# Optimization experiments

Measured on AMD Instinct MI355X. Metric: run time of the kernel, lower is better.

## Reference

```python
import jax, jax.numpy as jnp
import numpy as np
from jax import lax

KSIZE, STRIDE, RATE, SOFTMAX_SCALE = 3, 1, 2, 10.0


def extract_patches(x, k, stride):
    # x: [B,C,H,W] -> [B,C,k,k,oh,ow]; torch-style zero 'same' padding
    B, C, H, W = x.shape
    oh, ow = -(-H // stride), -(-W // stride)
    ph = max(0, (oh - 1) * stride + k - H)
    pw = max(0, (ow - 1) * stride + k - W)
    x = jnp.pad(x, ((0, 0), (0, 0), (ph // 2, ph - ph // 2), (pw // 2, pw - pw // 2)))
    cols = [x[:, :, i:i + (oh - 1) * stride + 1:stride, j:j + (ow - 1) * stride + 1:stride]
            for i in range(k) for j in range(k)]
    return jnp.stack(cols, axis=2).reshape(B, C, k, k, oh, ow)


def setup_inputs():
    key = jax.random.key(0)
    kf, kb = jax.random.split(key)
    f = jax.random.normal(kf, (2, 128, 128, 128), dtype=jnp.float32)
    b = jax.random.normal(kb, (2, 128, 128, 128), dtype=jnp.float32)
    mask = jnp.zeros((2, 1, 512, 512), dtype=jnp.float32)
    mask = mask.at[:, :, 128:384, 128:384].set(1.0)  # central hole: bg patches unavailable
    return {"f": f, "b": b, "mask": mask}


def reference(f, b, mask):
    B, C, H, W = b.shape
    kernel = 2 * RATE
    # raw background patches used for reconstruction (stride = rate*stride)
    raw = extract_patches(b, kernel, RATE * STRIDE)            # [B,C,4,4,Hb,Wb]
    Hb, Wb = raw.shape[-2:]
    L = Hb * Wb
    raw_w = raw.transpose(0, 4, 5, 1, 2, 3).reshape(B, L, C, kernel, kernel)
    # nearest 1/rate downsample (integer rate -> strided slice)
    fs = f[:, :, ::RATE, ::RATE]
    bs = b[:, :, ::RATE, ::RATE]
    Hf, Wf = fs.shape[-2:]
    # matching patches from downsampled background, L2-normalized per patch
    wp = extract_patches(bs, KSIZE, STRIDE)                    # [B,C,3,3,Hb,Wb]
    w = wp.transpose(0, 4, 5, 1, 2, 3).reshape(B, L, C, KSIZE, KSIZE)
    norm = jnp.sqrt(jnp.sum(w * w, axis=(2, 3, 4), keepdims=True))
    w_normed = w / jnp.maximum(norm, 1e-4)
    # mask -> per-patch validity (original uses batch element 0 only)
    ms = mask[:, :, ::4 * RATE, ::4 * RATE]                    # [B,1,Hb,Wb]
    mp = extract_patches(ms, KSIZE, STRIDE)[0]                 # [1,3,3,Hb,Wb]
    mm = (jnp.mean(mp, axis=(0, 1, 2)).reshape(-1) == 0.0).astype(f.dtype)
    mm = mm.reshape(1, L, 1, 1)
    # similarity scores: per-image conv2d of fg with bg patches == patch einsum
    fp = extract_patches(fs, KSIZE, STRIDE)                    # [B,C,3,3,Hf,Wf]
    yi = jnp.einsum('bcpqhw,blcpq->blhw', fp, w_normed)        # [B,L,Hf,Wf]
    yi = yi * mm
    yi = jax.nn.softmax(yi * SOFTMAX_SCALE, axis=1)
    yi = yi * mm
    # argmax offsets relative to reference coordinates (int_bs == int_fs here)
    off = jnp.argmax(yi, axis=1)                               # [B,Hf,Wf]
    h_ref = jnp.arange(Hf)[None, :, None]
    w_ref = jnp.arange(Wf)[None, None, :]
    offsets = jnp.stack([off // Wf - h_ref, off % Wf - w_ref], axis=1)  # [B,2,Hf,Wf]
    # reconstruction: conv_transpose2d(yi, raw_wi, stride=rate, padding=1) / 4
    w_ct = jnp.flip(raw_w.transpose(0, 2, 1, 3, 4), axis=(-2, -1))      # [B,C,L,4,4]
    pad = kernel - 1 - 1  # transpose-conv padding=1 -> conv pad k-1-1
    def ct(a, wk):
        return lax.conv_general_dilated(a[None], wk, (1, 1),
                                        ((pad, pad), (pad, pad)),
                                        lhs_dilation=(RATE, RATE),
                                        dimension_numbers=('NCHW', 'OIHW', 'NCHW'))[0]
    y = jax.vmap(ct)(yi, w_ct) / 4.0                           # [B,C,H,W]
    return y, offsets
```

## Files before the change

kernel.cpp:

```cpp
#include <hip/hip_runtime.h>
#include <hip/hip_bf16.h>
#include <cstdint>

#define B_  2
#define C_  128
#define HH  128
#define WW  128
#define L_  4096
#define K1  1152
#define M2  2048
#define NPAD 3072
#define NCAND 16
#define MARGIN 0.15f
#define PCUT 5e-4f
#define MAXC 512

typedef __attribute__((ext_vector_type(8))) short bf16x8s;
typedef __attribute__((ext_vector_type(4))) float f32x4;
typedef __attribute__((ext_vector_type(2))) float f32x2;
using bf16 = __hip_bfloat16;

__device__ inline float bf16bits2f(unsigned short s) {
  uint32_t u = ((uint32_t)s) << 16;
  return __builtin_bit_cast(float, u);
}
__device__ inline unsigned short f2bf16bits(float x) {
  uint32_t u = __builtin_bit_cast(uint32_t, x);
  u += 0x7fffu + ((u >> 16) & 1u);
  return (unsigned short)(u >> 16);
}

__device__ inline uint8_t fp8_encode(float v) {
  uint32_t s = (__builtin_bit_cast(uint32_t, v) >> 24) & 0x80u;
  float av = fabsf(v);
  uint32_t byte;
  if (av >= 0.015625f) {
    uint32_t bits = __builtin_bit_cast(uint32_t, av);
    uint32_t mant = bits & 0x7fffffu;
    uint32_t E = bits >> 23;
    uint32_t m3 = (mant + 0x7ffffu + ((mant >> 20) & 1u)) >> 20;
    if (m3 == 8u) { m3 = 0u; E++; }
    int e8 = (int)E - 120;
    if (e8 > 15) { e8 = 15; m3 = 6; }
    byte = ((uint32_t)e8 << 3) | m3;
  } else {
    byte = (uint32_t)(av * 512.f + 0.5f);
  }
  return (uint8_t)(s | byte);
}

#if __has_builtin(__builtin_amdgcn_cvt_pk_f32_fp8)
#define FP8PK(d, hi) __builtin_amdgcn_cvt_pk_f32_fp8((d), (hi))
#else
__device__ inline f32x2 FP8PK(uint32_t d, bool hi) {
  uint32_t b0 = hi ? ((d >> 16) & 0xffu) : (d & 0xffu);
  uint32_t b1 = hi ? (d >> 24) : ((d >> 8) & 0xffu);
  f32x2 r;
  r.x = __builtin_bit_cast(float, ((b0 & 0x80u) << 24) | ((b0 & 0x7fu) << 20)) * 0x1p120f;
  r.y = __builtin_bit_cast(float, ((b1 & 0x80u) << 24) | ((b1 & 0x7fu) << 20)) * 0x1p120f;
  return r;
}
#endif

__device__ inline void gload_lds16(const void* g, void* l) {
  auto gp = reinterpret_cast<const __attribute__((address_space(1))) uint32_t*>(
      reinterpret_cast<uintptr_t>(g));
  auto lp = reinterpret_cast<__attribute__((address_space(3))) uint32_t*>(
      reinterpret_cast<uintptr_t>(l));
  __builtin_amdgcn_global_load_lds(gp, lp, 16, 0, 0);
}

__global__ void compute_mm_k(const float* __restrict__ mask, float* __restrict__ mm) {
  int l = blockIdx.x * 256 + threadIdx.x;
  if (l >= L_) return;
  int i = l >> 6, j = l & 63;
  float s = 0.f;
  for (int p = -1; p <= 1; ++p)
    for (int q = -1; q <= 1; ++q) {
      int y = i + p, x = j + q;
      if ((unsigned)y < 64u && (unsigned)x < 64u)
        s += mask[(size_t)(8 * y) * 512 + 8 * x];
    }
  mm[l] = (s == 0.f) ? 1.f : 0.f;
}

__global__ __launch_bounds__(256) void compact_k(const float* __restrict__ mm,
                                                 int* __restrict__ vlist,
                                                 int* __restrict__ vmap,
                                                 int* __restrict__ meta) {
  __shared__ int wpart[4];
  int t = threadIdx.x;
  int lane = t & 63, wid = t >> 6;
  int loc[16];
  int cnt = 0;
#pragma unroll
  for (int s = 0; s < 16; ++s) {
    int l = t * 16 + s;
    loc[s] = cnt;
    cnt += (mm[l] != 0.f) ? 1 : 0;
  }
  int pre = cnt;
#pragma unroll
  for (int o = 1; o < 64; o <<= 1) {
    int u = __shfl_up(pre, o);
    if (lane >= o) pre += u;
  }
  if (lane == 63) wpart[wid] = pre;
  int excl = pre - cnt;
  __syncthreads();
  int base = 0;
  for (int w = 0; w < wid; ++w) base += wpart[w];
  int mybase = base + excl;
#pragma unroll
  for (int s = 0; s < 16; ++s) {
    int l = t * 16 + s;
    if (mm[l] != 0.f) {
      int pos = mybase + loc[s];
      vlist[pos] = l;
      vmap[l] = pos;
    }
  }
  if (t == 0) {
    int total = wpart[0] + wpart[1] + wpart[2] + wpart[3];
    meta[0] = total;
    meta[1] = L_ - total;
  }
}

__global__ __launch_bounds__(256) void prep_u_k(const float* __restrict__ bsrc,
                                                const float* __restrict__ mm,
                                                const int* __restrict__ vmap,
                                                bf16* __restrict__ Ucomp,
                                                float* __restrict__ U32) {
  __shared__ float red[4];
  int l = blockIdx.x;
  int bi = blockIdx.y;
  if (mm[l] == 0.f) return;
  int pos = vmap[l];
  int i = l >> 6, j = l & 63;
  int t = threadIdx.x;
  float vals[5];
  float ss = 0.f;
#pragma unroll
  for (int s = 0; s < 5; ++s) {
    int k = t + s * 256;
    float v = 0.f;
    if (k < K1) {
      int c = k / 9, r = k - c * 9;
      int p = r / 3, q = r - p * 3;
      int y = i + p - 1, x = j + q - 1;
      if ((unsigned)y < 64u && (unsigned)x < 64u)
        v = bsrc[(((size_t)bi * C_ + c) * HH + 2 * y) * WW + 2 * x];
    }
    vals[s] = v;
    ss += v * v;
  }
#pragma unroll
  for (int o = 32; o; o >>= 1) ss += __shfl_xor(ss, o);
  if ((t & 63) == 0) red[t >> 6] = ss;
  __syncthreads();
  float tot = red[0] + red[1] + red[2] + red[3];
  float den = fmaxf(sqrtf(tot), 1e-4f);
  float inv = 1.f / den;
  size_t cbase = ((size_t)bi * NPAD + pos) * K1;
  size_t obase = ((size_t)bi * L_ + l) * K1;
#pragma unroll
  for (int s = 0; s < 5; ++s) {
    int k = t + s * 256;
    if (k < K1) {
      float u = vals[s] * inv;
      Ucomp[cbase + k] = __float2bfloat16(u);
      U32[obase + k] = u;
    }
  }
}

__global__ __launch_bounds__(256) void prep_fp_k(const float* __restrict__ f,
                                                 bf16* __restrict__ FP,
                                                 float* __restrict__ FP32) {
  int idx = blockIdx.x * 256 + threadIdx.x;
  int bi = blockIdx.y;
  if (idx >= L_ * K1) return;
  int hw = idx / K1, k = idx - hw * K1;
  int h = hw >> 6, w = hw & 63;
  int c = k / 9, r = k - c * 9;
  int p = r / 3, q = r - p * 3;
  int y = h + p - 1, x = w + q - 1;
  float v = 0.f;
  if ((unsigned)y < 64u && (unsigned)x < 64u)
    v = f[(((size_t)bi * C_ + c) * HH + 2 * y) * WW + 2 * x];
  size_t o = (size_t)bi * L_ * K1 + idx;
  FP[o] = __float2bfloat16(v);
  FP32[o] = v;
}

__global__ void prep_bmatT_k(const float* __restrict__ bsrc, uint8_t* __restrict__ BmT8) {
  int idx = blockIdx.x * 256 + threadIdx.x;
  int bi = blockIdx.y;
  if (idx >= M2 * L_) return;
  int l = idx >> 11, m = idx & 2047;
  int c = m >> 4, p = (m >> 2) & 3, q = m & 3;
  int i = l >> 6, j = l & 63;
  int y = 2 * i + p - 1, x = 2 * j + q - 1;
  float v = 0.f;
  if ((unsigned)y < 128u && (unsigned)x < 128u)
    v = bsrc[(((size_t)bi * C_ + c) * HH + y) * WW + x];
  BmT8[(size_t)bi * M2 * L_ + idx] = fp8_encode(v);
}

__global__ __launch_bounds__(256) void gemm_bt(const bf16* __restrict__ A,
                                               const bf16* __restrict__ Bbase,
                                               bf16* __restrict__ C,
                                               int N, int K) {
  __shared__ __align__(16) bf16 sA[2][128][32];
  __shared__ __align__(16) bf16 sB[2][128][32];
  const int tid = threadIdx.x;
  const int lane = tid & 63;
  const int wid = tid >> 6;
  const int bm = blockIdx.x * 128;
  const int bn = blockIdx.y * 128;
  const bf16* B = Bbase + (size_t)(bm >> 12) * NPAD * K1;
  const int wm = (wid >> 1) * 64;
  const int wn = (wid & 1) * 64;
  const int lrow = lane & 15;
  const int lko = (lane >> 4) * 8;

  f32x4 acc[4][4];
#pragma unroll
  for (int i = 0; i < 4; ++i)
#pragma unroll
    for (int j = 0; j < 4; ++j) acc[i][j] = (f32x4){0.f, 0.f, 0.f, 0.f};

  const int nt = K >> 5;
  const int s0 = tid, s1 = tid + 256;
  const int ar0 = s0 >> 2, ac0 = (s0 & 3) * 8;
  const int ar1 = s1 >> 2, ac1 = (s1 & 3) * 8;

  auto STAGE = [&](int bufi, int t) {
    const int k0 = t * 32;
    gload_lds16(A + (size_t)(bm + ar0) * K + k0 + ac0, &sA[bufi][ar0][ac0]);
    gload_lds16(A + (size_t)(bm + ar1) * K + k0 + ac1, &sA[bufi][ar1][ac1]);
    gload_lds16(B + (size_t)(bn + ar0) * K + k0 + ac0, &sB[bufi][ar0][ac0]);
    gload_lds16(B + (size_t)(bn + ar1) * K + k0 + ac1, &sB[bufi][ar1][ac1]);
  };

  STAGE(0, 0);
  __syncthreads();
  int buf = 0;
  for (int t = 0; t < nt; ++t) {
    if (t + 1 < nt) STAGE(buf ^ 1, t + 1);
    bf16x8s af[4], bfr[4];
#pragma unroll
    for (int fm = 0; fm < 4; ++fm)
      af[fm] = *(const bf16x8s*)&sA[buf][wm + fm * 16 + lrow][lko];
#pragma unroll
    for (int fn = 0; fn < 4; ++fn)
      bfr[fn] = *(const bf16x8s*)&sB[buf][wn + fn * 16 + lrow][lko];
#pragma unroll
    for (int fm = 0; fm < 4; ++fm)
#pragma unroll
      for (int fn = 0; fn < 4; ++fn)
        acc[fm][fn] = __builtin_amdgcn_mfma_f32_16x16x32_bf16(af[fm], bfr[fn], acc[fm][fn], 0, 0, 0);
    __syncthreads();
    buf ^= 1;
  }

  const int crow = (lane >> 4) * 4;
  const int ccol = lane & 15;
#pragma unroll
  for (int fm = 0; fm < 4; ++fm)
#pragma unroll
    for (int fn = 0; fn < 4; ++fn) {
      int r0 = bm + wm + fm * 16 + crow;
      int c0 = bn + wn + fn * 16 + ccol;
#pragma unroll
      for (int r = 0; r < 4; ++r)
        C[(size_t)(r0 + r) * N + c0] = __float2bfloat16(acc[fm][fn][r]);
    }
}

__global__ __launch_bounds__(256) void softmax_spmv_k(const bf16* __restrict__ Sb,
                                                      const int* __restrict__ vlist,
                                                      const int* __restrict__ meta,
                                                      const uint8_t* __restrict__ BmT8b,
                                                      unsigned short* __restrict__ Ztb,
                                                      int* __restrict__ candb,
                                                      int* __restrict__ candcntb) {
  __shared__ float rmax[4];
  __shared__ float rsum[4];
  __shared__ int scnt, mcnt;
  __shared__ int slist[MAXC];
  __shared__ float splist[MAXC];
  __shared__ int mlist[NCAND];
  const int row = blockIdx.x;
  const int bi = blockIdx.y;
  const int t = threadIdx.x;
  const int vcnt = meta[0];
  const int nmask = meta[1];
  const uint8_t* BmT8 = BmT8b + (size_t)bi * M2 * L_;
  if (t == 0) { scnt = 0; mcnt = 0; }
  const bool has = (t < NPAD / 16);
  const int c0 = t * 16;
  float xs[16];
#pragma unroll
  for (int s = 0; s < 16; ++s) xs[s] = -1e30f;
  if (has) {
    const bf16* srow = Sb + ((size_t)bi * L_ + row) * NPAD;
    bf16x8s sv0 = *(const bf16x8s*)&srow[c0];
    bf16x8s sv1 = *(const bf16x8s*)&srow[c0 + 8];
#pragma unroll
    for (int s = 0; s < 8; ++s) {
      xs[s] = bf16bits2f((unsigned short)sv0[s]);
      xs[s + 8] = bf16bits2f((unsigned short)sv1[s]);
    }
  }
  float vmax = -1e30f;
#pragma unroll
  for (int s = 0; s < 16; ++s)
    if (has && c0 + s < vcnt) vmax = fmaxf(vmax, xs[s]);
#pragma unroll
  for (int o = 32; o; o >>= 1) vmax = fmaxf(vmax, __shfl_xor(vmax, o));
  if ((t & 63) == 0) rmax[t >> 6] = vmax;
  __syncthreads();
  vmax = fmaxf(fmaxf(rmax[0], rmax[1]), fmaxf(rmax[2], rmax[3]));
  float gmax = (nmask > 0) ? fmaxf(vmax, 0.f) : vmax;
  float zs = 0.f;
#pragma unroll
  for (int s = 0; s < 16; ++s)
    if (has && c0 + s < vcnt) zs += __expf(10.f * (xs[s] - gmax));
#pragma unroll
  for (int o = 32; o; o >>= 1) zs += __shfl_xor(zs, o);
  if ((t & 63) == 0) rsum[t >> 6] = zs;
  __syncthreads();
  zs = rsum[0] + rsum[1] + rsum[2] + rsum[3] + (float)nmask * __expf(-10.f * gmax);
  float invZ = 1.f / zs;
  float cutx = gmax + __logf(PCUT * zs) * 0.1f;
  if (has) {
#pragma unroll
    for (int s = 0; s < 16; ++s) {
      int c = c0 + s;
      if (c < vcnt) {
        if (xs[s] >= cutx) {
          int pos = atomicAdd(&scnt, 1);
          if (pos < MAXC) {
            slist[pos] = vlist[c];
            splist[pos] = __expf(10.f * (xs[s] - gmax)) * invZ;
          }
        }
        if (xs[s] >= vmax - MARGIN) {
          int pos = atomicAdd(&mcnt, 1);
          if (pos < NCAND) mlist[pos] = vlist[c];
        }
      }
    }
  }
  __syncthreads();
  int nc = min(scnt, MAXC);
  float acc[8] = {0.f, 0.f, 0.f, 0.f, 0.f, 0.f, 0.f, 0.f};
#pragma unroll 4
  for (int ci = 0; ci < nc; ++ci) {
    int l = slist[ci];
    float p = splist[ci];
    const uint32_t* bp = (const uint32_t*)(BmT8 + (size_t)l * M2) + t * 2;
    uint32_t d0 = bp[0], d1 = bp[1];
    f32x2 w0 = FP8PK(d0, false);
    f32x2 w1 = FP8PK(d0, true);
    f32x2 w2 = FP8PK(d1, false);
    f32x2 w3 = FP8PK(d1, true);
    acc[0] += p * w0.x; acc[1] += p * w0.y;
    acc[2] += p * w1.x; acc[3] += p * w1.y;
    acc[4] += p * w2.x; acc[5] += p * w2.y;
    acc[6] += p * w3.x; acc[7] += p * w3.y;
  }
  bf16x8s zv;
#pragma unroll
  for (int j = 0; j < 8; ++j) zv[j] = (short)f2bf16bits(acc[j]);
  *(bf16x8s*)&Ztb[((size_t)bi * L_ + row) * M2 + t * 8] = zv;
  if (t == 0) candcntb[bi * L_ + row] = min(mcnt, NCAND);
  if (t < NCAND && t < mcnt) candb[(bi * L_ + row) * NCAND + t] = mlist[t];
}

__global__ __launch_bounds__(256) void transpose_k(const unsigned short* __restrict__ inb,
                                                   unsigned short* __restrict__ outb) {
  __shared__ ushort2 tile[32][33];
  int bi = blockIdx.z;
  const unsigned short* in = inb + (size_t)bi * L_ * M2;
  unsigned short* out = outb + (size_t)bi * M2 * L_;
  int bm2 = blockIdx.x * 32;
  int bh = blockIdx.y * 32;
  int tx = threadIdx.x & 31;
  int ty = threadIdx.x >> 5;
  const ushort2* in2 = (const ushort2*)in;
#pragma unroll
  for (int r = 0; r < 32; r += 8)
    tile[ty + r][tx] = in2[(size_t)(bh + ty + r) * (M2 / 2) + bm2 + tx];
  __syncthreads();
#pragma unroll
  for (int r = 0; r < 32; r += 8) {
    ushort2 v = tile[tx][ty + r];
    int mp = bm2 + ty + r;
    out[(size_t)(2 * mp) * L_ + bh + tx] = v.x;
    out[(size_t)(2 * mp + 1) * L_ + bh + tx] = v.y;
  }
}

__global__ __launch_bounds__(256) void rescore_k(const float* __restrict__ FP32b,
                                                 const float* __restrict__ U32b,
                                                 const int* __restrict__ candb,
                                                 const int* __restrict__ candcntb,
                                                 float* __restrict__ offout) {
  __shared__ float red[4];
  const int row = blockIdx.x;
  const int bi = blockIdx.y;
  const int t = threadIdx.x;
  const int h = row >> 6, w = row & 63;
  const float* FP32 = FP32b + (size_t)bi * L_ * K1;
  const float* U32 = U32b + (size_t)bi * L_ * K1;
  const int* cand = candb + (size_t)(bi * L_ + row) * NCAND;
  int cnt = candcntb[bi * L_ + row];
  int bestl;
  if (cnt <= 1) {
    bestl = cand[0];
  } else {
    float fv[5];
#pragma unroll
    for (int s = 0; s < 5; ++s) {
      int k = t + s * 256;
      fv[s] = (k < K1) ? FP32[(size_t)row * K1 + k] : 0.f;
    }
    float bestv = -1e30f;
    bestl = 0x7fffffff;
    for (int ci = 0; ci < cnt; ++ci) {
      int l = cand[ci];
      const float* urow = U32 + (size_t)l * K1;
      float dot = 0.f;
#pragma unroll
      for (int s = 0; s < 5; ++s) {
        int k = t + s * 256;
        if (k < K1) dot += fv[s] * urow[k];
      }
#pragma unroll
      for (int o = 32; o; o >>= 1) dot += __shfl_xor(dot, o);
      if ((t & 63) == 0) red[t >> 6] = dot;
      __syncthreads();
      dot = red[0] + red[1] + red[2] + red[3];
      if (dot > bestv || (dot == bestv && l < bestl)) { bestv = dot; bestl = l; }
      __syncthreads();
    }
  }
  if (t == 0) {
    int istar = bestl >> 6, jstar = bestl & 63;
    offout[(size_t)bi * 8192 + row] = (float)(istar - h);
    offout[(size_t)bi * 8192 + L_ + row] = (float)(jstar - w);
  }
}

__global__ void gather_k(const unsigned short* __restrict__ Z2b, float* __restrict__ yout) {
  int u = blockIdx.x, c = blockIdx.y, bi = blockIdx.z;
  int t = threadIdx.x;
  const unsigned short* Z2 = Z2b + (size_t)bi * M2 * L_;
  int h0 = (u + 1) >> 1, p0 = (u + 1) & 1;
  int h1 = h0 - 1, p1 = p0 + 2;
  float a0 = 0.f, a1 = 0.f;
#pragma unroll
  for (int e = 0; e < 2; ++e) {
    int h = e ? h1 : h0;
    int p = e ? p1 : p0;
    if ((unsigned)h < 64u) {
      const unsigned short* zb = Z2 + (size_t)(c * 16 + p * 4) * L_ + h * 64;
      a0 += bf16bits2f(zb[1 * L_ + t]);
      if (t >= 1) a0 += bf16bits2f(zb[3 * L_ + (t - 1)]);
      if (t < 63) a1 += bf16bits2f(zb[0 * L_ + (t + 1)]);
      a1 += bf16bits2f(zb[2 * L_ + t]);
    }
  }
  size_t ybase = (((size_t)bi * C_ + c) * HH + u) * WW;
  yout[ybase + 2 * t] = a0 * 0.25f;
  yout[ybase + 2 * t + 1] = a1 * 0.25f;
}

extern "C" void kernel_launch(void* const* d_in, const int* in_sizes, int n_in,
                              void* d_out, int out_size, void* d_ws, size_t ws_size,
                              hipStream_t stream) {
  const float* f = (const float*)d_in[0];
  const float* b = (const float*)d_in[1];
  const float* mask = (const float*)d_in[2];
  float* out = (float*)d_out;
  char* ws = (char*)d_ws;

  size_t off = 0;
  float* mm = (float*)(ws + off);          off += 16384;
  int* vlist = (int*)(ws + off);           off += 16384;
  int* vmap = (int*)(ws + off);            off += 16384;
  int* meta = (int*)(ws + off);            off += 16384;
  int* cand = (int*)(ws + off);            off += (size_t)B_ * L_ * NCAND * 4;
  int* candcnt = (int*)(ws + off);         off += 65536;
  bf16* Ucomp = (bf16*)(ws + off);         off += (size_t)B_ * NPAD * K1 * 2;
  bf16* FP = (bf16*)(ws + off);            off += (size_t)B_ * L_ * K1 * 2;
  float* U32 = (float*)(ws + off);         off += (size_t)B_ * L_ * K1 * 4;
  float* FP32 = (float*)(ws + off);        off += (size_t)B_ * L_ * K1 * 4;
  uint8_t* BmT8 = (uint8_t*)(ws + off);    off += (size_t)B_ * M2 * L_;
  bf16* S = (bf16*)(ws + off);             off += (size_t)B_ * L_ * NPAD * 2;
  unsigned short* Zt = (unsigned short*)(ws + off); off += (size_t)B_ * M2 * L_ * 2;
  unsigned short* Z2 = (unsigned short*)(ws + off); off += (size_t)B_ * M2 * L_ * 2;
  float* yout = out;
  float* offout = out + (size_t)B_ * C_ * HH * WW;

  compute_mm_k<<<16, 256, 0, stream>>>(mask, mm);
  compact_k<<<1, 256, 0, stream>>>(mm, vlist, vmap, meta);
  prep_u_k<<<dim3(L_, B_), 256, 0, stream>>>(b, mm, vmap, Ucomp, U32);
  prep_fp_k<<<dim3((L_ * K1 + 255) / 256, B_), 256, 0, stream>>>(f, FP, FP32);
  prep_bmatT_k<<<dim3((M2 * L_ + 255) / 256, B_), 256, 0, stream>>>(b, BmT8);
  gemm_bt<<<dim3(B_ * L_ / 128, NPAD / 128), 256, 0, stream>>>(FP, Ucomp, S, NPAD, K1);
  softmax_spmv_k<<<dim3(L_, B_), 256, 0, stream>>>(S, vlist, meta, BmT8, Zt, cand, candcnt);
  rescore_k<<<dim3(L_, B_), 256, 0, stream>>>(FP32, U32, cand, candcnt, offout);
  transpose_k<<<dim3(M2 / 64, L_ / 32, B_), 256, 0, stream>>>(Zt, Z2);
  gather_k<<<dim3(128, 128, B_), 64, 0, stream>>>(Z2, yout);
}
```

Baseline: 256.9 us.

## Fuse mask and prep kernels, swizzle GEMM tiles, widen gather blocks, raise PCUT

```diff
diff --git a/kernel.cpp b/kernel.cpp
--- a/kernel.cpp
+++ b/kernel.cpp
@@ -12,7 +12,7 @@
 #define NPAD 3072
 #define NCAND 16
 #define MARGIN 0.15f
-#define PCUT 5e-4f
+#define PCUT 1e-3f
 #define MAXC 512
 
 typedef __attribute__((ext_vector_type(8))) short bf16x8s;
@@ -70,21 +70,8 @@
   __builtin_amdgcn_global_load_lds(gp, lp, 16, 0, 0);
 }
 
-__global__ void compute_mm_k(const float* __restrict__ mask, float* __restrict__ mm) {
-  int l = blockIdx.x * 256 + threadIdx.x;
-  if (l >= L_) return;
-  int i = l >> 6, j = l & 63;
-  float s = 0.f;
-  for (int p = -1; p <= 1; ++p)
-    for (int q = -1; q <= 1; ++q) {
-      int y = i + p, x = j + q;
-      if ((unsigned)y < 64u && (unsigned)x < 64u)
-        s += mask[(size_t)(8 * y) * 512 + 8 * x];
-    }
-  mm[l] = (s == 0.f) ? 1.f : 0.f;
-}
-
-__global__ __launch_bounds__(256) void compact_k(const float* __restrict__ mm,
+__global__ __launch_bounds__(256) void compact_k(const float* __restrict__ mask,
+                                                 float* __restrict__ mm,
                                                  int* __restrict__ vlist,
                                                  int* __restrict__ vmap,
                                                  int* __restrict__ meta) {
@@ -92,12 +79,23 @@
   int t = threadIdx.x;
   int lane = t & 63, wid = t >> 6;
   int loc[16];
+  float mmv[16];
   int cnt = 0;
 #pragma unroll
   for (int s = 0; s < 16; ++s) {
     int l = t * 16 + s;
+    int i = l >> 6, j = l & 63;
+    float sum = 0.f;
+    for (int p = -1; p <= 1; ++p)
+      for (int q = -1; q <= 1; ++q) {
+        int y = i + p, x = j + q;
+        if ((unsigned)y < 64u && (unsigned)x < 64u)
+          sum += mask[(size_t)(8 * y) * 512 + 8 * x];
+      }
+    mmv[s] = (sum == 0.f) ? 1.f : 0.f;
+    mm[l] = mmv[s];
     loc[s] = cnt;
-    cnt += (mm[l] != 0.f) ? 1 : 0;
+    cnt += (mmv[s] != 0.f) ? 1 : 0;
   }
   int pre = cnt;
 #pragma unroll
@@ -114,7 +112,7 @@
 #pragma unroll
   for (int s = 0; s < 16; ++s) {
     int l = t * 16 + s;
-    if (mm[l] != 0.f) {
+    if (mmv[s] != 0.f) {
       int pos = mybase + loc[s];
       vlist[pos] = l;
       vmap[l] = pos;
@@ -127,85 +125,89 @@
   }
 }
 
-__global__ __launch_bounds__(256) void prep_u_k(const float* __restrict__ bsrc,
-                                                const float* __restrict__ mm,
-                                                const int* __restrict__ vmap,
-                                                bf16* __restrict__ Ucomp,
-                                                float* __restrict__ U32) {
-  __shared__ float red[4];
-  int l = blockIdx.x;
-  int bi = blockIdx.y;
-  if (mm[l] == 0.f) return;
-  int pos = vmap[l];
-  int i = l >> 6, j = l & 63;
+#define PU_BLKS (B_ * L_)
+#define PF_BLKS (B_ * L_ * K1 / 256)
+#define PB_BLKS (B_ * M2 * L_ / 256)
+__global__ __launch_bounds__(256) void prep_all_k(const float* __restrict__ f,
+                                                  const float* __restrict__ b,
+                                                  const float* __restrict__ mm,
+                                                  const int* __restrict__ vmap,
+                                                  bf16* __restrict__ Ucomp,
+                                                  float* __restrict__ U32,
+                                                  bf16* __restrict__ FP,
+                                                  float* __restrict__ FP32,
+                                                  uint8_t* __restrict__ BmT8) {
+  int bx = blockIdx.x;
   int t = threadIdx.x;
-  float vals[5];
-  float ss = 0.f;
-#pragma unroll
-  for (int s = 0; s < 5; ++s) {
-    int k = t + s * 256;
+  if (bx < PU_BLKS) {
+    __shared__ float red[4];
+    int l = bx & (L_ - 1);
+    int bi = bx >> 12;
+    if (mm[l] == 0.f) return;
+    int pos = vmap[l];
+    int i = l >> 6, j = l & 63;
+    float vals[5];
+    float ss = 0.f;
+#pragma unroll
+    for (int s = 0; s < 5; ++s) {
+      int k = t + s * 256;
+      float v = 0.f;
+      if (k < K1) {
+        int c = k / 9, r = k - c * 9;
+        int p = r / 3, q = r - p * 3;
+        int y = i + p - 1, x = j + q - 1;
+        if ((unsigned)y < 64u && (unsigned)x < 64u)
+          v = b[(((size_t)bi * C_ + c) * HH + 2 * y) * WW + 2 * x];
+      }
+      vals[s] = v;
+      ss += v * v;
+    }
+#pragma unroll
+    for (int o = 32; o; o >>= 1) ss += __shfl_xor(ss, o);
+    if ((t & 63) == 0) red[t >> 6] = ss;
+    __syncthreads();
+    float tot = red[0] + red[1] + red[2] + red[3];
+    float den = fmaxf(sqrtf(tot), 1e-4f);
+    float inv = 1.f / den;
+    size_t cbase = ((size_t)bi * NPAD + pos) * K1;
+    size_t obase = ((size_t)bi * L_ + l) * K1;
+#pragma unroll
+    for (int s = 0; s < 5; ++s) {
+      int k = t + s * 256;
+      if (k < K1) {
+        float u = vals[s] * inv;
+        Ucomp[cbase + k] = __float2bfloat16(u);
+        U32[obase + k] = u;
+      }
+    }
+  } else if (bx < PU_BLKS + PF_BLKS) {
+    int gidx = (bx - PU_BLKS) * 256 + t;
+    int bi = gidx / (L_ * K1);
+    int idx = gidx - bi * (L_ * K1);
+    int hw = idx / K1, k = idx - hw * K1;
+    int h = hw >> 6, w = hw & 63;
+    int c = k / 9, r = k - c * 9;
+    int p = r / 3, q = r - p * 3;
+    int y = h + p - 1, x = w + q - 1;
     float v = 0.f;
-    if (k < K1) {
-      int c = k / 9, r = k - c * 9;
-      int p = r / 3, q = r - p * 3;
-      int y = i + p - 1, x = j + q - 1;
-      if ((unsigned)y < 64u && (unsigned)x < 64u)
-        v = bsrc[(((size_t)bi * C_ + c) * HH + 2 * y) * WW + 2 * x];
-    }
-    vals[s] = v;
-    ss += v * v;
-  }
-#pragma unroll
-  for (int o = 32; o; o >>= 1) ss += __shfl_xor(ss, o);
-  if ((t & 63) == 0) red[t >> 6] = ss;
-  __syncthreads();
-  float tot = red[0] + red[1] + red[2] + red[3];
-  float den = fmaxf(sqrtf(tot), 1e-4f);
-  float inv = 1.f / den;
-  size_t cbase = ((size_t)bi * NPAD + pos) * K1;
-  size_t obase = ((size_t)bi * L_ + l) * K1;
-#pragma unroll
-  for (int s = 0; s < 5; ++s) {
-    int k = t + s * 256;
-    if (k < K1) {
-      float u = vals[s] * inv;
-      Ucomp[cbase + k] = __float2bfloat16(u);
-      U32[obase + k] = u;
-    }
-  }
-}
-
-__global__ __launch_bounds__(256) void prep_fp_k(const float* __restrict__ f,
-                                                 bf16* __restrict__ FP,
-                                                 float* __restrict__ FP32) {
-  int idx = blockIdx.x * 256 + threadIdx.x;
-  int bi = blockIdx.y;
-  if (idx >= L_ * K1) return;
-  int hw = idx / K1, k = idx - hw * K1;
-  int h = hw >> 6, w = hw & 63;
-  int c = k / 9, r = k - c * 9;
-  int p = r / 3, q = r - p * 3;
-  int y = h + p - 1, x = w + q - 1;
-  float v = 0.f;
-  if ((unsigned)y < 64u && (unsigned)x < 64u)
-    v = f[(((size_t)bi * C_ + c) * HH + 2 * y) * WW + 2 * x];
-  size_t o = (size_t)bi * L_ * K1 + idx;
-  FP[o] = __float2bfloat16(v);
-  FP32[o] = v;
-}
-
-__global__ void prep_bmatT_k(const float* __restrict__ bsrc, uint8_t* __restrict__ BmT8) {
-  int idx = blockIdx.x * 256 + threadIdx.x;
-  int bi = blockIdx.y;
-  if (idx >= M2 * L_) return;
-  int l = idx >> 11, m = idx & 2047;
-  int c = m >> 4, p = (m >> 2) & 3, q = m & 3;
-  int i = l >> 6, j = l & 63;
-  int y = 2 * i + p - 1, x = 2 * j + q - 1;
-  float v = 0.f;
-  if ((unsigned)y < 128u && (unsigned)x < 128u)
-    v = bsrc[(((size_t)bi * C_ + c) * HH + y) * WW + x];
-  BmT8[(size_t)bi * M2 * L_ + idx] = fp8_encode(v);
+    if ((unsigned)y < 64u && (unsigned)x < 64u)
+      v = f[(((size_t)bi * C_ + c) * HH + 2 * y) * WW + 2 * x];
+    size_t o = (size_t)gidx;
+    FP[o] = __float2bfloat16(v);
+    FP32[o] = v;
+  } else {
+    int gidx = (bx - PU_BLKS - PF_BLKS) * 256 + t;
+    int bi = gidx >> 23;
+    int idx = gidx & (M2 * L_ - 1);
+    int l = idx >> 11, m = idx & 2047;
+    int c = m >> 4, p = (m >> 2) & 3, q = m & 3;
+    int i = l >> 6, j = l & 63;
+    int y = 2 * i + p - 1, x = 2 * j + q - 1;
+    float v = 0.f;
+    if ((unsigned)y < 128u && (unsigned)x < 128u)
+      v = b[(((size_t)bi * C_ + c) * HH + y) * WW + x];
+    BmT8[(size_t)gidx] = fp8_encode(v);
+  }
 }
 
 __global__ __launch_bounds__(256) void gemm_bt(const bf16* __restrict__ A,
@@ -214,11 +216,13 @@
                                                int N, int K) {
   __shared__ __align__(16) bf16 sA[2][128][32];
   __shared__ __align__(16) bf16 sB[2][128][32];
+  const int wg = blockIdx.x;
+  const int swz = (wg & 7) * 192 + (wg >> 3);
+  const int bm = (swz & 63) * 128;
+  const int bn = (swz >> 6) * 128;
   const int tid = threadIdx.x;
   const int lane = tid & 63;
   const int wid = tid >> 6;
-  const int bm = blockIdx.x * 128;
-  const int bn = blockIdx.y * 128;
   const bf16* B = Bbase + (size_t)(bm >> 12) * NPAD * K1;
   const int wm = (wid >> 1) * 64;
   const int wn = (wid & 1) * 64;
@@ -455,9 +459,11 @@
   }
 }
 
-__global__ void gather_k(const unsigned short* __restrict__ Z2b, float* __restrict__ yout) {
-  int u = blockIdx.x, c = blockIdx.y, bi = blockIdx.z;
-  int t = threadIdx.x;
+__global__ __launch_bounds__(256) void gather_k(const unsigned short* __restrict__ Z2b,
+                                                float* __restrict__ yout) {
+  int c = blockIdx.y, bi = blockIdx.z;
+  int t = threadIdx.x & 63;
+  int u = blockIdx.x * 4 + (threadIdx.x >> 6);
   const unsigned short* Z2 = Z2b + (size_t)bi * M2 * L_;
   int h0 = (u + 1) >> 1, p0 = (u + 1) & 1;
   int h1 = h0 - 1, p1 = p0 + 2;
@@ -506,14 +512,12 @@
   float* yout = out;
   float* offout = out + (size_t)B_ * C_ * HH * WW;
 
-  compute_mm_k<<<16, 256, 0, stream>>>(mask, mm);
-  compact_k<<<1, 256, 0, stream>>>(mm, vlist, vmap, meta);
-  prep_u_k<<<dim3(L_, B_), 256, 0, stream>>>(b, mm, vmap, Ucomp, U32);
-  prep_fp_k<<<dim3((L_ * K1 + 255) / 256, B_), 256, 0, stream>>>(f, FP, FP32);
-  prep_bmatT_k<<<dim3((M2 * L_ + 255) / 256, B_), 256, 0, stream>>>(b, BmT8);
-  gemm_bt<<<dim3(B_ * L_ / 128, NPAD / 128), 256, 0, stream>>>(FP, Ucomp, S, NPAD, K1);
+  compact_k<<<1, 256, 0, stream>>>(mask, mm, vlist, vmap, meta);
+  prep_all_k<<<PU_BLKS + PF_BLKS + PB_BLKS, 256, 0, stream>>>(f, b, mm, vmap, Ucomp, U32,
+                                                              FP, FP32, BmT8);
+  gemm_bt<<<1536, 256, 0, stream>>>(FP, Ucomp, S, NPAD, K1);
   softmax_spmv_k<<<dim3(L_, B_), 256, 0, stream>>>(S, vlist, meta, BmT8, Zt, cand, candcnt);
   rescore_k<<<dim3(L_, B_), 256, 0, stream>>>(FP32, U32, cand, candcnt, offout);
   transpose_k<<<dim3(M2 / 64, L_ / 32, B_), 256, 0, stream>>>(Zt, Z2);
-  gather_k<<<dim3(128, 128, B_), 64, 0, stream>>>(Z2, yout);
-}
+  gather_k<<<dim3(32, 128, B_), 256, 0, stream>>>(Z2, yout);
+}
```

After: 280.8 us. +9.3%, slower.

## Fuse mask validity into compaction, widen gather blocks, raise softmax prob cutoff

Applied to the files above, without the earlier changes.

```diff
diff --git a/kernel.cpp b/kernel.cpp
--- a/kernel.cpp
+++ b/kernel.cpp
@@ -12,7 +12,7 @@
 #define NPAD 3072
 #define NCAND 16
 #define MARGIN 0.15f
-#define PCUT 5e-4f
+#define PCUT 1e-3f
 #define MAXC 512
 
 typedef __attribute__((ext_vector_type(8))) short bf16x8s;
@@ -70,21 +70,8 @@
   __builtin_amdgcn_global_load_lds(gp, lp, 16, 0, 0);
 }
 
-__global__ void compute_mm_k(const float* __restrict__ mask, float* __restrict__ mm) {
-  int l = blockIdx.x * 256 + threadIdx.x;
-  if (l >= L_) return;
-  int i = l >> 6, j = l & 63;
-  float s = 0.f;
-  for (int p = -1; p <= 1; ++p)
-    for (int q = -1; q <= 1; ++q) {
-      int y = i + p, x = j + q;
-      if ((unsigned)y < 64u && (unsigned)x < 64u)
-        s += mask[(size_t)(8 * y) * 512 + 8 * x];
-    }
-  mm[l] = (s == 0.f) ? 1.f : 0.f;
-}
-
-__global__ __launch_bounds__(256) void compact_k(const float* __restrict__ mm,
+__global__ __launch_bounds__(256) void compact_k(const float* __restrict__ mask,
+                                                 float* __restrict__ mm,
                                                  int* __restrict__ vlist,
                                                  int* __restrict__ vmap,
                                                  int* __restrict__ meta) {
@@ -92,12 +79,23 @@
   int t = threadIdx.x;
   int lane = t & 63, wid = t >> 6;
   int loc[16];
+  float mmv[16];
   int cnt = 0;
 #pragma unroll
   for (int s = 0; s < 16; ++s) {
     int l = t * 16 + s;
+    int i = l >> 6, j = l & 63;
+    float sum = 0.f;
+    for (int p = -1; p <= 1; ++p)
+      for (int q = -1; q <= 1; ++q) {
+        int y = i + p, x = j + q;
+        if ((unsigned)y < 64u && (unsigned)x < 64u)
+          sum += mask[(size_t)(8 * y) * 512 + 8 * x];
+      }
+    mmv[s] = (sum == 0.f) ? 1.f : 0.f;
+    mm[l] = mmv[s];
     loc[s] = cnt;
-    cnt += (mm[l] != 0.f) ? 1 : 0;
+    cnt += (mmv[s] != 0.f) ? 1 : 0;
   }
   int pre = cnt;
 #pragma unroll
@@ -114,7 +112,7 @@
 #pragma unroll
   for (int s = 0; s < 16; ++s) {
     int l = t * 16 + s;
-    if (mm[l] != 0.f) {
+    if (mmv[s] != 0.f) {
       int pos = mybase + loc[s];
       vlist[pos] = l;
       vmap[l] = pos;
@@ -455,9 +453,11 @@
   }
 }
 
-__global__ void gather_k(const unsigned short* __restrict__ Z2b, float* __restrict__ yout) {
-  int u = blockIdx.x, c = blockIdx.y, bi = blockIdx.z;
-  int t = threadIdx.x;
+__global__ __launch_bounds__(256) void gather_k(const unsigned short* __restrict__ Z2b,
+                                                float* __restrict__ yout) {
+  int c = blockIdx.y, bi = blockIdx.z;
+  int t = threadIdx.x & 63;
+  int u = blockIdx.x * 4 + (threadIdx.x >> 6);
   const unsigned short* Z2 = Z2b + (size_t)bi * M2 * L_;
   int h0 = (u + 1) >> 1, p0 = (u + 1) & 1;
   int h1 = h0 - 1, p1 = p0 + 2;
@@ -506,8 +506,7 @@
   float* yout = out;
   float* offout = out + (size_t)B_ * C_ * HH * WW;
 
-  compute_mm_k<<<16, 256, 0, stream>>>(mask, mm);
-  compact_k<<<1, 256, 0, stream>>>(mm, vlist, vmap, meta);
+  compact_k<<<1, 256, 0, stream>>>(mask, mm, vlist, vmap, meta);
   prep_u_k<<<dim3(L_, B_), 256, 0, stream>>>(b, mm, vmap, Ucomp, U32);
   prep_fp_k<<<dim3((L_ * K1 + 255) / 256, B_), 256, 0, stream>>>(f, FP, FP32);
   prep_bmatT_k<<<dim3((M2 * L_ + 255) / 256, B_), 256, 0, stream>>>(b, BmT8);
@@ -515,5 +514,5 @@
   softmax_spmv_k<<<dim3(L_, B_), 256, 0, stream>>>(S, vlist, meta, BmT8, Zt, cand, candcnt);
   rescore_k<<<dim3(L_, B_), 256, 0, stream>>>(FP32, U32, cand, candcnt, offout);
   transpose_k<<<dim3(M2 / 64, L_ / 32, B_), 256, 0, stream>>>(Zt, Z2);
-  gather_k<<<dim3(128, 128, B_), 64, 0, stream>>>(Z2, yout);
-}
+  gather_k<<<dim3(32, 128, B_), 256, 0, stream>>>(Z2, yout);
+}
```

Measured after the change: 276.4 us. 1.08x slower.
